# Kernel tuning notes

Measured on AMD Instinct MI355X. Metric: run time of the kernel, lower is better.

Reference implementation:

```python
import jax, jax.numpy as jnp
import numpy as np

N_NODES = 10000
N_EDGES = 320000
N_REL = 460
N_BASES = 30
D = 200


def setup_inputs() -> dict:
    key = jax.random.key(0)
    k = jax.random.split(key, 8)
    x = jax.random.normal(k[0], (N_NODES, D), dtype=jnp.float32)
    edge_index = jax.random.randint(k[1], (2, N_EDGES), 0, N_NODES, dtype=jnp.int32)
    edge_type = jax.random.randint(k[2], (N_EDGES,), 0, N_REL, dtype=jnp.int32)
    # Xavier-uniform-like init scales
    w_bound = float(np.sqrt(6.0 / (D + D)))
    c_bound = float(np.sqrt(6.0 / (N_REL + N_BASES)))
    weight = jax.random.uniform(k[3], (N_BASES, D, D), minval=-w_bound, maxval=w_bound, dtype=jnp.float32)
    coeff = jax.random.uniform(k[4], (N_REL, N_BASES), minval=-c_bound, maxval=c_bound, dtype=jnp.float32)
    self_weight = jax.random.uniform(k[5], (D, D), minval=-w_bound, maxval=w_bound, dtype=jnp.float32)
    bias = jnp.zeros((D,), dtype=jnp.float32)
    return {
        "x": x,
        "weight": weight,
        "coeff": coeff,
        "self_weight": self_weight,
        "bias": bias,
        "edge_index": edge_index,
        "edge_type": edge_type,
        "num_nodes": N_NODES,
    }


def reference(x, weight, coeff, self_weight, bias, edge_index, edge_type, num_nodes):
    # RelationalGraphConv.forward:
    #   W_r = sum_b coeff[r, b] * V_b ; msg_e = x[src_e] @ W_{type_e}
    #   out[n] = (sum_{e: tgt_e = n} msg_e) / max(in_deg[n], 1) + x @ W_self + bias
    src = edge_index[0]
    tgt = edge_index[1]
    src_feats = x[src]                    # (E, d_in) gather
    edge_coeff = coeff[edge_type]         # (E, B) gather

    # msg_e = sum_b coeff[type_e, b] * (src_e @ V_b): scan over bases to avoid
    # materializing an (E, B, d_out) intermediate (same math as W_r = coeff @ V).
    def body(acc, inputs):
        Vb, cb = inputs                   # (d_in, d_out), (E,)
        return acc + (src_feats @ Vb) * cb[:, None], None

    msg0 = jnp.zeros((src.shape[0], weight.shape[2]), dtype=x.dtype)
    msg, _ = jax.lax.scan(body, msg0, (weight, edge_coeff.T))  # (E, d_out)

    out = jax.ops.segment_sum(msg, tgt, num_segments=num_nodes)              # (N, d_out)
    deg = jax.ops.segment_sum(jnp.ones_like(tgt, dtype=x.dtype), tgt, num_segments=num_nodes)
    out = out / jnp.clip(deg, 1.0)[:, None]
    out = out + x @ self_weight + bias
    return out
```

## Files before the change

### kernel.cpp

```cpp
#include <hip/hip_runtime.h>
#include <hip/hip_bf16.h>

#define N_NODES 10000
#define N_EDGES 320000
#define N_REL   460
#define N_BASES 30
#define DIM     200
#define KZ      6016
#define KT      6240
#define NSTEPS  195
#define NTILES  313
#define NFRAG   16
#define KSPLIT  6
#define PROWS   10016

using short8  = __attribute__((ext_vector_type(8))) short;
using floatx4 = __attribute__((ext_vector_type(4))) float;

__device__ __forceinline__ unsigned short f2bf(float f) {
    union { float f; unsigned u; } v; v.f = f;
    unsigned u = v.u;
    return (unsigned short)((u + 0x7fffu + ((u >> 16) & 1u)) >> 16);
}

__device__ __forceinline__ short8 pack8(const unsigned short* u) {
    union { unsigned short s[8]; short8 v; } p;
#pragma unroll
    for (int i = 0; i < 8; ++i) p.s[i] = u[i];
    return p.v;
}

__device__ __forceinline__ size_t asw_idx(int n, int c) {
    int t = n >> 5, half = (n >> 4) & 1, rl = n & 15;
    int kk = c >> 5, w = c & 31;
    return (((size_t)(t * NSTEPS + kk) * 2 + half) * 16 + rl) * 32 + w;
}


__global__ void hist_kernel(const int* tgt, int* deg) {
    int e = blockIdx.x * blockDim.x + threadIdx.x;
    if (e < N_EDGES) atomicAdd(&deg[tgt[e]], 1);
}

__global__ __launch_bounds__(1024) void scan_kernel(const int* deg, int* starts,
                                                    int* cursor, float* dinv) {
    __shared__ int part[1024];
    int tid = threadIdx.x;
    const int PER = (N_NODES + 1023) / 1024;
    int base = tid * PER;
    int s = 0;
    for (int i = 0; i < PER; ++i) { int idx = base + i; if (idx < N_NODES) s += deg[idx]; }
    part[tid] = s; __syncthreads();
    for (int off = 1; off < 1024; off <<= 1) {
        int v = (tid >= off) ? part[tid - off] : 0;
        __syncthreads();
        part[tid] += v;
        __syncthreads();
    }
    int run = (tid > 0) ? part[tid - 1] : 0;
    for (int i = 0; i < PER; ++i) {
        int idx = base + i;
        if (idx < N_NODES) {
            int d = deg[idx];
            starts[idx] = run; cursor[idx] = run;
            dinv[idx] = 1.0f / (float)(d > 0 ? d : 1);
            run += d;
        }
    }
    if (tid == 1023) starts[N_NODES] = part[1023];
}

__global__ void scatter_kernel(const int* src, const int* tgt, const int* etype,
                               int* cursor, int2* sedge) {
    int e = blockIdx.x * blockDim.x + threadIdx.x;
    if (e < N_EDGES) {
        int t = tgt[e];
        int pos = atomicAdd(&cursor[t], 1);
        sedge[pos] = make_int2(src[e], etype[e]);
    }
}


__global__ void fill_b_kernel(const float* weight, const float* sw, unsigned short* BSW) {
    int idx = blockIdx.x * blockDim.x + threadIdx.x;
    if (idx >= NFRAG * NSTEPS * 512) return;
    int f = idx / (NSTEPS * 512);
    int rem = idx - f * (NSTEPS * 512);
    int kk = rem / 512;
    int e = rem - kk * 512;
    int l = e >> 3, j = e & 7;
    int rB = f * 16 + (l & 15);
    int k  = kk * 32 + (l >> 4) * 8 + j;
    float v = 0.f;
    if (rB < DIM) {
        if (k < KZ) {
            if (k < N_BASES * DIM) {
                int b = k / DIM, kc = k - b * DIM;
                v = weight[(b * DIM + kc) * DIM + rB];
            }
        } else {
            int jj = k - KZ;
            if (jj < DIM) v = sw[jj * DIM + rB];
        }
    }
    BSW[idx] = f2bf(v);
}

__global__ void fill_x_kernel(const float* x, const int* deg,
                              unsigned short* Xbf, unsigned short* ASW) {
    int idx = blockIdx.x * blockDim.x + threadIdx.x;
    if (idx >= N_NODES * 224) return;
    int n = idx / 224, j = idx - n * 224;
    float v = (j < DIM) ? x[(size_t)n * DIM + j] : 0.f;
    if (j < DIM) Xbf[(size_t)n * DIM + j] = f2bf(v);
    int d = deg[n]; if (d < 1) d = 1;
    ASW[asw_idx(n, KZ + j)] = f2bf((float)d * v);
}

__global__ void fill_cpair_kernel(const float* coeff, unsigned int* Cpair) {
    int idx = blockIdx.x * blockDim.x + threadIdx.x;
    if (idx >= N_REL * 16) return;
    int t = idx >> 4, m = idx & 15;
    unsigned lo = f2bf(coeff[t * N_BASES + m]);
    unsigned hi = (m + 16 < N_BASES) ? f2bf(coeff[t * N_BASES + m + 16]) : 0u;
    Cpair[idx] = lo | (hi << 16);
}


__global__ __launch_bounds__(256) void agg_kernel(const unsigned short* __restrict__ Xbf,
                                                  const unsigned int* __restrict__ Cpair,
                                                  const int* __restrict__ starts,
                                                  const int2* __restrict__ sedge,
                                                  unsigned short* __restrict__ ASW) {
    __shared__ __align__(16) unsigned short zbuf[4][3232];
    int lane = threadIdx.x & 63;
    int wave = threadIdx.x >> 6;
    int n = blockIdx.x * 4 + wave;
    int ln = lane & 15, q = lane >> 4;

    floatx4 acc0[13], acc1[13];
#pragma unroll
    for (int f = 0; f < 13; ++f) {
        acc0[f] = (floatx4){0.f, 0.f, 0.f, 0.f};
        acc1[f] = acc0[f];
    }

    int e0 = starts[n], e1 = starts[n + 1];
    for (int kb = e0; kb < e1; kb += 32) {
        int eb = kb + 8 * q;
        unsigned short a0v[8], a1v[8];
        int srcs[8];
#pragma unroll
        for (int j = 0; j < 8; ++j) {
            int e = eb + j;
            int ec = (e < e1) ? e : (e1 - 1);
            int2 sd = sedge[ec];
            unsigned cp = (e < e1) ? Cpair[sd.y * 16 + ln] : 0u;
            a0v[j] = (unsigned short)(cp & 0xffffu);
            a1v[j] = (unsigned short)(cp >> 16);
            srcs[j] = sd.x;
        }
        short8 A0 = pack8(a0v), A1 = pack8(a1v);

        unsigned short bv[2][8];
#pragma unroll
        for (int j = 0; j < 8; ++j)
            bv[0][j] = Xbf[(size_t)srcs[j] * DIM + ln];
#pragma unroll
        for (int f = 0; f < 13; ++f) {
            int cur = f & 1, nxt = cur ^ 1;
            if (f < 12) {
#pragma unroll
                for (int j = 0; j < 8; ++j)
                    bv[nxt][j] = Xbf[(size_t)srcs[j] * DIM + (f + 1) * 16 + ln];
            }
            short8 B = pack8(bv[cur]);
            acc0[f] = __builtin_amdgcn_mfma_f32_16x16x32_bf16(A0, B, acc0[f], 0, 0, 0);
            acc1[f] = __builtin_amdgcn_mfma_f32_16x16x32_bf16(A1, B, acc1[f], 0, 0, 0);
        }
    }

    unsigned short* zb = zbuf[wave];
    int t = n >> 5, half = (n >> 4) & 1, rl = n & 15;
    const uint4* zb4 = (const uint4*)zb;
    uint4* dst = (uint4*)ASW;
    size_t base_u4 = ((size_t)t * NSTEPS * 2 + half) * 64 + rl * 4;

#pragma unroll
    for (int f = 0; f < 13; ++f) {
        int d = f * 16 + ln;
        if (d < DIM) {
#pragma unroll
            for (int i = 0; i < 4; ++i)
                zb[(q * 4 + i) * DIM + d] = f2bf(acc0[f][i]);
        }
    }
    for (int v = lane; v < 400; v += 64) {
        int kk = v >> 2, w8 = v & 3;
        dst[base_u4 + (size_t)kk * 128 + w8] = zb4[v];
    }

    if (lane < 16) zb[2800 + lane] = 0;
#pragma unroll
    for (int f = 0; f < 13; ++f) {
        int d = f * 16 + ln;
        if (d < DIM) {
#pragma unroll
            for (int i = 0; i < 4; ++i) {
                int b1 = 16 + q * 4 + i;
                if (b1 < N_BASES) zb[(b1 - 16) * DIM + d] = f2bf(acc1[f][i]);
            }
        }
    }
    for (int v = lane; v < 352; v += 64) {
        int kk = 100 + (v >> 2), w8 = v & 3;
        dst[base_u4 + (size_t)kk * 128 + w8] = zb4[v];
    }
}


__global__ __launch_bounds__(256) void gemm_kernel(const unsigned short* __restrict__ ASW,
                                                   const unsigned short* __restrict__ BSW,
                                                   float* __restrict__ part) {
    int tid = threadIdx.x;
    int lane = tid & 63, wave = tid >> 6;
    int tile = blockIdx.x, chunk = blockIdx.y;
    int ks = (chunk * NSTEPS) / KSPLIT;
    int ke = ((chunk + 1) * NSTEPS) / KSPLIT;
    int ln = lane & 15, q = lane >> 4;

    const unsigned short* pa = ASW + (size_t)tile * NSTEPS * 1024 + ln * 32 + q * 8;
    const unsigned short* pb = BSW + lane * 8;

    floatx4 acc0[4], acc1[4];
#pragma unroll
    for (int i = 0; i < 4; ++i) {
        acc0[i] = (floatx4){0.f, 0.f, 0.f, 0.f};
        acc1[i] = acc0[i];
    }

    for (int kk = ks; kk < ke; ++kk) {
        short8 a0 = *(const short8*)(pa + (size_t)kk * 1024);
        short8 a1 = *(const short8*)(pa + (size_t)kk * 1024 + 512);
#pragma unroll
        for (int i = 0; i < 4; ++i) {
            int f = wave + 4 * i;
            short8 b = *(const short8*)(pb + (size_t)(f * NSTEPS + kk) * 512);
            acc0[i] = __builtin_amdgcn_mfma_f32_16x16x32_bf16(a0, b, acc0[i], 0, 0, 0);
            acc1[i] = __builtin_amdgcn_mfma_f32_16x16x32_bf16(a1, b, acc1[i], 0, 0, 0);
        }
    }

    int row0 = tile * 32;
    float* pbase = part + ((size_t)chunk * PROWS + row0) * 208;
#pragma unroll
    for (int i = 0; i < 4; ++i) {
        int fg = wave + 4 * i;
        if (fg < 13) {
            int c = fg * 16 + ln;
#pragma unroll
            for (int ii = 0; ii < 4; ++ii) {
                pbase[(q * 4 + ii) * 208 + c]      = acc0[i][ii];
                pbase[(16 + q * 4 + ii) * 208 + c] = acc1[i][ii];
            }
        }
    }
}


__global__ __launch_bounds__(256) void reduce_kernel(const float* __restrict__ part,
                                                     const float* __restrict__ dinv,
                                                     const float* __restrict__ bias,
                                                     float* __restrict__ out) {
    int idx = blockIdx.x * blockDim.x + threadIdx.x;
    if (idx >= N_NODES * 50) return;
    int r = idx / 50, cq = idx - r * 50;
    float4 s = {0.f, 0.f, 0.f, 0.f};
#pragma unroll
    for (int c = 0; c < KSPLIT; ++c) {
        float4 v = *(const float4*)(part + ((size_t)c * PROWS + r) * 208 + cq * 4);
        s.x += v.x; s.y += v.y; s.z += v.z; s.w += v.w;
    }
    float dv = dinv[r];
    float4 b = *(const float4*)(bias + cq * 4);
    float4 o;
    o.x = s.x * dv + b.x; o.y = s.y * dv + b.y;
    o.z = s.z * dv + b.z; o.w = s.w * dv + b.w;
    *(float4*)(out + (size_t)r * DIM + cq * 4) = o;
}


extern "C" void kernel_launch(void* const* d_in, const int* in_sizes, int n_in,
                              void* d_out, int out_size, void* d_ws, size_t ws_size,
                              hipStream_t stream) {
    const float* x      = (const float*)d_in[0];
    const float* weight = (const float*)d_in[1];
    const float* coeff  = (const float*)d_in[2];
    const float* selfw  = (const float*)d_in[3];
    const float* bias   = (const float*)d_in[4];
    const int*   eidx   = (const int*)d_in[5];
    const int*   etype  = (const int*)d_in[6];
    const int* src = eidx;
    const int* tgt = eidx + N_EDGES;
    float* out = (float*)d_out;

    char* ws = (char*)d_ws;
    size_t off = 0;
    auto carve = [&](size_t bytes) {
        char* p = ws + off;
        off += (bytes + 255) & ~(size_t)255;
        return p;
    };
    unsigned short* ASW  = (unsigned short*)carve((size_t)NTILES * NSTEPS * 1024 * 2);
    unsigned short* BSW  = (unsigned short*)carve((size_t)NFRAG * NSTEPS * 512 * 2);
    float* part   = (float*)carve((size_t)KSPLIT * PROWS * 208 * 4);
    unsigned short* Xbf  = (unsigned short*)carve((size_t)(N_NODES * DIM + 64) * 2);
    unsigned int*  Cpair = (unsigned int*)carve((size_t)N_REL * 16 * 4);
    int*   deg    = (int*)carve((size_t)N_NODES * 4);
    int*   starts = (int*)carve((size_t)(N_NODES + 1) * 4);
    int*   cursor = (int*)carve((size_t)N_NODES * 4);
    float* dinv   = (float*)carve((size_t)N_NODES * 4);
    int2*  sedge  = (int2*)carve((size_t)N_EDGES * 8);

    hipMemsetAsync(deg, 0, (size_t)N_NODES * 4, stream);
    hist_kernel<<<(N_EDGES + 255) / 256, 256, 0, stream>>>(tgt, deg);
    scan_kernel<<<1, 1024, 0, stream>>>(deg, starts, cursor, dinv);
    scatter_kernel<<<(N_EDGES + 255) / 256, 256, 0, stream>>>(src, tgt, etype, cursor, sedge);

    fill_b_kernel<<<(NFRAG * NSTEPS * 512 + 255) / 256, 256, 0, stream>>>(weight, selfw, BSW);
    fill_x_kernel<<<(N_NODES * 224 + 255) / 256, 256, 0, stream>>>(x, deg, Xbf, ASW);
    fill_cpair_kernel<<<(N_REL * 16 + 255) / 256, 256, 0, stream>>>(coeff, Cpair);

    agg_kernel<<<N_NODES / 4, 256, 0, stream>>>(Xbf, Cpair, starts, sedge, ASW);

    dim3 ggrid(NTILES, KSPLIT);
    gemm_kernel<<<ggrid, 256, 0, stream>>>(ASW, BSW, part);

    reduce_kernel<<<(N_NODES * 50 + 255) / 256, 256, 0, stream>>>(part, dinv, bias, out);
}
```

Baseline: 277.3 us.

## Enlarge GEMM row tile to 64 and prefetch next K-step fragments

The swizzled A layout and GEMM tile go from 32 to 64 rows per tile, so each wave issues 16 MFMAs per K-step against 4 A fragments and reuses each B fragment four times instead of twice. The loop also loads the next K-step's A and B fragments into registers before running the current MFMAs, a software double-buffer meant to hide global load latency. This halves the number of tiles and blocks and raises accumulator register use, which may lower occupancy.

```diff
diff --git a/kernel.cpp b/kernel.cpp
--- a/kernel.cpp
+++ b/kernel.cpp
@@ -9,10 +9,11 @@
 #define KZ      6016
 #define KT      6240
 #define NSTEPS  195
-#define NTILES  313
+#define NTILES  157
 #define NFRAG   16
 #define KSPLIT  6
-#define PROWS   10016
+#define PROWS   10048
+#define TKELEM  2048
 
 using short8  = __attribute__((ext_vector_type(8))) short;
 using floatx4 = __attribute__((ext_vector_type(4))) float;
@@ -31,9 +32,9 @@
 }
 
 __device__ __forceinline__ size_t asw_idx(int n, int c) {
-    int t = n >> 5, half = (n >> 4) & 1, rl = n & 15;
+    int t = n >> 6, sub = (n >> 4) & 3, rl = n & 15;
     int kk = c >> 5, w = c & 31;
-    return (((size_t)(t * NSTEPS + kk) * 2 + half) * 16 + rl) * 32 + w;
+    return (size_t)(t * NSTEPS + kk) * TKELEM + sub * 512 + rl * 32 + w;
 }
 
 
@@ -181,10 +182,10 @@
     }
 
     unsigned short* zb = zbuf[wave];
-    int t = n >> 5, half = (n >> 4) & 1, rl = n & 15;
+    int t = n >> 6, sub = (n >> 4) & 3, rl = n & 15;
     const uint4* zb4 = (const uint4*)zb;
     uint4* dst = (uint4*)ASW;
-    size_t base_u4 = ((size_t)t * NSTEPS * 2 + half) * 64 + rl * 4;
+    size_t base_u4 = (size_t)t * NSTEPS * 256 + sub * 64 + rl * 4;
 
 #pragma unroll
     for (int f = 0; f < 13; ++f) {
@@ -197,7 +198,7 @@
     }
     for (int v = lane; v < 400; v += 64) {
         int kk = v >> 2, w8 = v & 3;
-        dst[base_u4 + (size_t)kk * 128 + w8] = zb4[v];
+        dst[base_u4 + (size_t)kk * 256 + w8] = zb4[v];
     }
 
     if (lane < 16) zb[2800 + lane] = 0;
@@ -214,7 +215,7 @@
     }
     for (int v = lane; v < 352; v += 64) {
         int kk = 100 + (v >> 2), w8 = v & 3;
-        dst[base_u4 + (size_t)kk * 128 + w8] = zb4[v];
+        dst[base_u4 + (size_t)kk * 256 + w8] = zb4[v];
     }
 }
 
@@ -229,29 +230,43 @@
     int ke = ((chunk + 1) * NSTEPS) / KSPLIT;
     int ln = lane & 15, q = lane >> 4;
 
-    const unsigned short* pa = ASW + (size_t)tile * NSTEPS * 1024 + ln * 32 + q * 8;
-    const unsigned short* pb = BSW + lane * 8;
-
-    floatx4 acc0[4], acc1[4];
-#pragma unroll
-    for (int i = 0; i < 4; ++i) {
-        acc0[i] = (floatx4){0.f, 0.f, 0.f, 0.f};
-        acc1[i] = acc0[i];
-    }
+    const unsigned short* pa = ASW + (size_t)tile * NSTEPS * TKELEM + ln * 32 + q * 8;
+    const unsigned short* pbf[4];
+#pragma unroll
+    for (int i = 0; i < 4; ++i)
+        pbf[i] = BSW + (size_t)((wave + 4 * i) * NSTEPS) * 512 + lane * 8;
+
+    floatx4 acc[4][4];
+#pragma unroll
+    for (int i = 0; i < 4; ++i)
+#pragma unroll
+        for (int s = 0; s < 4; ++s) acc[i][s] = (floatx4){0.f, 0.f, 0.f, 0.f};
+
+    short8 a[4], b[4];
+#pragma unroll
+    for (int s = 0; s < 4; ++s) a[s] = *(const short8*)(pa + (size_t)ks * TKELEM + s * 512);
+#pragma unroll
+    for (int i = 0; i < 4; ++i) b[i] = *(const short8*)(pbf[i] + (size_t)ks * 512);
 
     for (int kk = ks; kk < ke; ++kk) {
-        short8 a0 = *(const short8*)(pa + (size_t)kk * 1024);
-        short8 a1 = *(const short8*)(pa + (size_t)kk * 1024 + 512);
-#pragma unroll
-        for (int i = 0; i < 4; ++i) {
-            int f = wave + 4 * i;
-            short8 b = *(const short8*)(pb + (size_t)(f * NSTEPS + kk) * 512);
-            acc0[i] = __builtin_amdgcn_mfma_f32_16x16x32_bf16(a0, b, acc0[i], 0, 0, 0);
-            acc1[i] = __builtin_amdgcn_mfma_f32_16x16x32_bf16(a1, b, acc1[i], 0, 0, 0);
-        }
-    }
-
-    int row0 = tile * 32;
+        int kn = (kk + 1 < ke) ? kk + 1 : kk;
+        short8 an[4], bn[4];
+#pragma unroll
+        for (int s = 0; s < 4; ++s) an[s] = *(const short8*)(pa + (size_t)kn * TKELEM + s * 512);
+#pragma unroll
+        for (int i = 0; i < 4; ++i) bn[i] = *(const short8*)(pbf[i] + (size_t)kn * 512);
+#pragma unroll
+        for (int i = 0; i < 4; ++i)
+#pragma unroll
+            for (int s = 0; s < 4; ++s)
+                acc[i][s] = __builtin_amdgcn_mfma_f32_16x16x32_bf16(a[s], b[i], acc[i][s], 0, 0, 0);
+#pragma unroll
+        for (int s = 0; s < 4; ++s) a[s] = an[s];
+#pragma unroll
+        for (int i = 0; i < 4; ++i) b[i] = bn[i];
+    }
+
+    int row0 = tile * 64;
     float* pbase = part + ((size_t)chunk * PROWS + row0) * 208;
 #pragma unroll
     for (int i = 0; i < 4; ++i) {
@@ -259,10 +274,10 @@
         if (fg < 13) {
             int c = fg * 16 + ln;
 #pragma unroll
-            for (int ii = 0; ii < 4; ++ii) {
-                pbase[(q * 4 + ii) * 208 + c]      = acc0[i][ii];
-                pbase[(16 + q * 4 + ii) * 208 + c] = acc1[i][ii];
-            }
+            for (int s = 0; s < 4; ++s)
+#pragma unroll
+                for (int ii = 0; ii < 4; ++ii)
+                    pbase[(s * 16 + q * 4 + ii) * 208 + c] = acc[i][s][ii];
         }
     }
 }
@@ -311,7 +326,7 @@
         off += (bytes + 255) & ~(size_t)255;
         return p;
     };
-    unsigned short* ASW  = (unsigned short*)carve((size_t)NTILES * NSTEPS * 1024 * 2);
+    unsigned short* ASW  = (unsigned short*)carve((size_t)NTILES * NSTEPS * TKELEM * 2);
     unsigned short* BSW  = (unsigned short*)carve((size_t)NFRAG * NSTEPS * 512 * 2);
     float* part   = (float*)carve((size_t)KSPLIT * PROWS * 208 * 4);
     unsigned short* Xbf  = (unsigned short*)carve((size_t)(N_NODES * DIM + 64) * 2);
```

New measurement: 262.3 us. -5.4%, faster.
